# Performance work log

Hardware: AMD Instinct MI355X
Metric: run time of the kernel (lower is better)

## Reference

```python
import jax, jax.numpy as jnp
import numpy as np


def _conv(x, w, b, stride=1):
    # torch Conv2d(kernel=3, padding=1) in NCHW / OIHW layout
    y = jax.lax.conv_general_dilated(x, w, (stride, stride), ((1, 1), (1, 1)),
                                     dimension_numbers=('NCHW', 'OIHW', 'NCHW'))
    return y + b[None, :, None, None]


def _up2(x):
    # nn.Upsample(scale_factor=2, mode='nearest')
    return jnp.repeat(jnp.repeat(x, 2, axis=2), 2, axis=3)


def _decode(z, fc_w, fc_b, w1, b1, w2, b2, w3, b3):
    # ConvDecoderMid: fc -> [B,32,7,7] -> up -> elu(conv) -> up -> elu(conv) -> sigmoid(conv)
    B = z.shape[0]
    h = (z @ fc_w + fc_b).reshape(B, 32, 7, 7)
    h = _up2(h)
    h = jax.nn.elu(_conv(h, w1, b1))
    h = _up2(h)
    h = jax.nn.elu(_conv(h, w2, b2))
    return jax.nn.sigmoid(_conv(h, w3, b3))  # [B,1,28,28]


def setup_inputs() -> dict:
    key = jax.random.key(0)
    B, L, E = 2048, 64, 8
    ks = jax.random.split(key, 16)
    rn = lambda k, s, sc: jax.random.normal(k, s, dtype=jnp.float32) * sc
    p = {}
    p['x'] = jax.random.uniform(ks[0], (B, 1, 28, 28), dtype=jnp.float32)
    p['eps'] = jax.random.normal(ks[1], (B, L), dtype=jnp.float32)
    # ConvEncoder
    p['enc_w1'] = rn(ks[2], (32, 1, 3, 3), 0.3);  p['enc_b1'] = jnp.zeros((32,), jnp.float32)
    p['enc_w2'] = rn(ks[3], (64, 32, 3, 3), 0.06); p['enc_b2'] = jnp.zeros((64,), jnp.float32)
    p['enc_w3'] = rn(ks[4], (128, 64, 3, 3), 0.04); p['enc_b3'] = jnp.zeros((128,), jnp.float32)
    p['w_mu'] = rn(ks[5], (128 * 7 * 7, L), 0.01); p['b_mu'] = jnp.zeros((L,), jnp.float32)
    p['w_lv'] = rn(ks[6], (128 * 7 * 7, L), 0.01); p['b_lv'] = jnp.zeros((L,), jnp.float32)
    # GatingNetwork
    p['g_w1'] = rn(ks[7], (L, 64), 0.1); p['g_b1'] = jnp.zeros((64,), jnp.float32)
    p['g_w2'] = rn(ks[8], (64, 32), 0.1); p['g_b2'] = jnp.zeros((32,), jnp.float32)
    p['g_w3'] = rn(ks[9], (32, E), 0.1); p['g_b3'] = jnp.zeros((E,), jnp.float32)
    # E ConvDecoderMid experts, params stacked on leading expert axis
    p['d_fc_w'] = rn(ks[10], (E, L, 32 * 7 * 7), 0.05); p['d_fc_b'] = jnp.zeros((E, 32 * 7 * 7), jnp.float32)
    p['d_w1'] = rn(ks[11], (E, 64, 32, 3, 3), 0.06); p['d_b1'] = jnp.zeros((E, 64), jnp.float32)
    p['d_w2'] = rn(ks[12], (E, 32, 64, 3, 3), 0.04); p['d_b2'] = jnp.zeros((E, 32), jnp.float32)
    p['d_w3'] = rn(ks[13], (E, 1, 32, 3, 3), 0.06); p['d_b3'] = jnp.zeros((E, 1), jnp.float32)
    return p


def reference(x, eps, enc_w1, enc_b1, enc_w2, enc_b2, enc_w3, enc_b3,
              w_mu, b_mu, w_lv, b_lv,
              g_w1, g_b1, g_w2, g_b2, g_w3, g_b3,
              d_fc_w, d_fc_b, d_w1, d_b1, d_w2, d_b2, d_w3, d_b3):
    B = x.shape[0]
    # encoder: 28 -> 28 -> 14 -> 7
    h = jax.nn.relu(_conv(x, enc_w1, enc_b1))
    h = jax.nn.relu(_conv(h, enc_w2, enc_b2, stride=2))
    h = jax.nn.relu(_conv(h, enc_w3, enc_b3, stride=2))
    h = h.reshape(B, -1)  # [B, 6272]
    mu = h @ w_mu + b_mu
    log_var = h @ w_lv + b_lv
    z = mu + eps * jnp.exp(0.5 * log_var)
    # gating
    g = jax.nn.relu(z @ g_w1 + g_b1)
    g = jax.nn.relu(g @ g_w2 + g_b2)
    expert_probs = jax.nn.softmax(g @ g_w3 + g_b3, axis=-1)
    expert_indices = jnp.argmax(expert_probs, axis=-1)  # [B]
    # run ALL experts on full batch (faithful to original), stack [E,B,1,28,28]
    all_rec = jax.vmap(_decode, in_axes=(None, 0, 0, 0, 0, 0, 0, 0, 0))(
        z, d_fc_w, d_fc_b, d_w1, d_b1, d_w2, d_b2, d_w3, d_b3)
    reconstructed_x = all_rec[expert_indices, jnp.arange(B)]  # [B,1,28,28]
    logits = jnp.log(expert_probs + 1e-8)
    return (reconstructed_x, mu, log_var, logits, expert_probs)
```

## Files before the change

kernel.cpp:

```cpp
#include <hip/hip_runtime.h>
#include <hip/hip_bf16.h>


#define NB 2048

typedef short bf16x8 __attribute__((ext_vector_type(8)));
typedef float f32x4  __attribute__((ext_vector_type(4)));
typedef unsigned u32x4 __attribute__((ext_vector_type(4)));

static constexpr int OFF_RECON  = 0;
static constexpr int OFF_MU     = 1605632;
static constexpr int OFF_LV     = 1736704;
static constexpr int OFF_LOGITS = 1867776;
static constexpr int OFF_PROBS  = 1884160;

static constexpr size_t WS_U    = 0;
static constexpr size_t WS_Z    = 25690112;
static constexpr size_t WS_IDX  = 25821184;
static constexpr size_t WS_WENC = 25821696;
static constexpr size_t W2S_OFF = 0;
static constexpr size_t W3S_OFF = 36864;
static constexpr size_t WFC_OFF = 184320;
static constexpr size_t HFC_OFF = 0;
static constexpr size_t W1B_OFF = 17000448;
static constexpr size_t WCB_OFF = 17074176;

__device__ __forceinline__ float relu_f(float v) { return v > 0.f ? v : 0.f; }
__device__ __forceinline__ float elu_f(float v)  {
  return __expf(fminf(v, 0.f)) - 1.f + fmaxf(v, 0.f);
}
__device__ __forceinline__ short f2b(float v) {
  __hip_bfloat16 h = __float2bfloat16(v);
  short s; __builtin_memcpy(&s, &h, 2); return s;
}
__device__ __forceinline__ float s2f(short s) {
  unsigned v = ((unsigned)(unsigned short)s) << 16;
  float f; __builtin_memcpy(&f, &v, 4); return f;
}
__device__ __forceinline__ unsigned pack2(float v) {
  short h = f2b(v);
  short m = f2b(v - s2f(h));
  return (unsigned)(unsigned short)h | ((unsigned)(unsigned short)m << 16);
}

__global__ __launch_bounds__(256) void k_prep_enc(
    const float* __restrict__ ew2, const float* __restrict__ ew3,
    const float* __restrict__ wmu, const float* __restrict__ wlv,
    unsigned short* __restrict__ w2s, unsigned short* __restrict__ w3s,
    unsigned* __restrict__ wfc)
{
  const int u = blockIdx.x * 256 + threadIdx.x;
  if (u >= 894976) return;
  if (u >= 92160) {
    const int u2 = u - 92160;
    const int kp = u2 >> 8, r = u2 & 255;
    const int n = r >> 1, j = r & 1;
    const int k = kp * 2 + j;
    const float w = (n < 64) ? wmu[k * 64 + n] : wlv[k * 64 + (n - 64)];
    short h = f2b(w);
    short mm = f2b(w - s2f(h));
    wfc[u2] = (unsigned)(unsigned short)h | ((unsigned)(unsigned short)mm << 16);
    return;
  }
  float w; uint2* dst;
  if (u < 18432) {
    int ic = u & 7, oc = (u >> 3) & 63;
    int r = u >> 9;
    int tap = r % 9, chunk = r / 9;
    w = ew2[oc * 288 + (chunk * 8 + ic) * 9 + tap];
    dst = (uint2*)w2s + u;
  } else {
    int u2 = u - 18432;
    int ic = u2 & 7, oc = (u2 >> 3) & 127;
    int r = u2 >> 10;
    int tap = r % 9, chunk = r / 9;
    w = ew3[oc * 576 + (chunk * 8 + ic) * 9 + tap];
    dst = (uint2*)w3s + u2;
  }
  short h = f2b(w);
  short mm = f2b(w - s2f(h));
  uint2 pk;
  pk.x = (unsigned)(unsigned short)h | ((unsigned)(unsigned short)mm << 16);
  pk.y = (unsigned)(unsigned short)h | ((unsigned)(unsigned short)h << 16);
  *dst = pk;
}

__global__ __launch_bounds__(512, 4) void k_enc(
    const float* __restrict__ x,
    const float* __restrict__ w1, const float* __restrict__ b1,
    const float* __restrict__ b2g, const unsigned short* __restrict__ w2s,
    const unsigned short* __restrict__ w3s, const float* __restrict__ b3,
    unsigned* __restrict__ hb)
{
  __shared__ float sX[900];
  __shared__ float sB2[64];
  __shared__ float sB3[128];
  __shared__ __align__(16) short sH[36000];

  const int n = blockIdx.x, t = threadIdx.x;

  for (int idx = t; idx < 900; idx += 512) {
    int yy = idx / 30, xx = idx % 30;
    float v = 0.f;
    if (yy >= 1 && yy <= 28 && xx >= 1 && xx <= 28)
      v = x[n * 784 + (yy - 1) * 28 + (xx - 1)];
    sX[idx] = v;
  }
  if (t < 64) sB2[t] = b2g[t];
  if (t >= 64 && t < 192) sB3[t - 64] = b3[t - 64];
  for (int bi = t; bi < 116; bi += 512) {
    int p;
    if (bi < 30) p = bi;
    else if (bi < 60) p = 870 + (bi - 30);
    else if (bi < 88) p = (bi - 59) * 30;
    else p = (bi - 87) * 30 + 29;
    unsigned* d = (unsigned*)&sH[p * 40];
    #pragma unroll
    for (int j = 0; j < 20; ++j) d[j] = 0u;
  }
  __syncthreads();

  float xw[2][9];
  int hp[2]; bool pvld[2];
  #pragma unroll
  for (int i = 0; i < 2; ++i) {
    int p = t + 512 * i;
    pvld[i] = (p < 784);
    int yy = pvld[i] ? p / 28 : 0, xx = pvld[i] ? p % 28 : 0;
    hp[i] = (yy + 1) * 30 + xx + 1;
    #pragma unroll
    for (int k = 0; k < 9; ++k)
      xw[i][k] = sX[(yy + k / 3) * 30 + xx + (k % 3)];
  }

  const int lane = t & 63, wv = t >> 6;
  const int q = lane >> 4, m16 = lane & 15;
  const int nth = wv & 1, mh = wv >> 1;
  const int nm = (mh == 0) ? 4 : 3;

  int abase[4];
  #pragma unroll
  for (int mtl = 0; mtl < 4; ++mtl) {
    int m = (mh + 4 * mtl) * 16 + m16; if (m > 195) m = 195;
    int yy = m / 14, xx = m % 14;
    abase[mtl] = (yy * 60 + xx * 2) * 40 + q * 8;
  }
  f32x4 acc[4][2];
  #pragma unroll
  for (int a = 0; a < 4; ++a) { acc[a][0] = (f32x4)0.f; acc[a][1] = (f32x4)0.f; }

  for (int c = 0; c < 4; ++c) {
    #pragma unroll
    for (int o = 0; o < 8; ++o) {
      const int oc = c * 8 + o;
      float wr[9];
      #pragma unroll
      for (int k = 0; k < 9; ++k) wr[k] = w1[oc * 9 + k];
      const float bb = b1[oc];
      #pragma unroll
      for (int i = 0; i < 2; ++i) if (pvld[i]) {
        float v = bb;
        #pragma unroll
        for (int k = 0; k < 9; ++k) v += xw[i][k] * wr[k];
        v = relu_f(v);
        short h = f2b(v); float hf = s2f(h);
        short mm = f2b(v - hf); float mf = s2f(mm);
        short ll = f2b(v - hf - mf);
        uint2 pk;
        pk.x = (unsigned)(unsigned short)h | ((unsigned)(unsigned short)h << 16);
        pk.y = (unsigned)(unsigned short)mm | ((unsigned)(unsigned short)ll << 16);
        *(uint2*)&sH[hp[i] * 40 + o * 4] = pk;
      }
    }
    __syncthreads();

    const unsigned short* wb = w2s + (size_t)c * 18432;
    for (int tap = 0; tap < 9; ++tap) {
      const int toff = ((tap / 3) * 30 + (tap % 3)) * 40;
      bf16x8 A[4];
      #pragma unroll
      for (int mtl = 0; mtl < 4; ++mtl)
        A[mtl] = *(const bf16x8*)&sH[abase[mtl] + toff];
      #pragma unroll
      for (int ntl = 0; ntl < 2; ++ntl) {
        const int ocl = nth * 32 + ntl * 16 + m16;
        bf16x8 B = *(const bf16x8*)&wb[(tap * 64 + ocl) * 32 + q * 8];
        #pragma unroll
        for (int mtl = 0; mtl < 4; ++mtl)
          if (mtl < nm)
            acc[mtl][ntl] = __builtin_amdgcn_mfma_f32_16x16x32_bf16(A[mtl], B, acc[mtl][ntl], 0, 0, 0);
      }
    }
    __syncthreads();
  }

  unsigned* h2p = (unsigned*)sH;
  short* sIn = sH + 25600;
  #pragma unroll
  for (int mtl = 0; mtl < 4; ++mtl) {
    if (mtl < nm) {
      const int mt = mh + 4 * mtl;
      #pragma unroll
      for (int ntl = 0; ntl < 2; ++ntl) {
        const int oc = nth * 32 + ntl * 16 + m16;
        const float bb = sB2[oc];
        #pragma unroll
        for (int r = 0; r < 4; ++r) {
          int p = mt * 16 + q * 4 + r;
          if (p < 196)
            h2p[p * 65 + oc] = pack2(relu_f(acc[mtl][ntl][r] + bb));
        }
      }
    }
  }
  for (int bi = t; bi < 60; bi += 512) {
    int p;
    if (bi < 16) p = bi;
    else if (bi < 32) p = 240 + (bi - 16);
    else if (bi < 46) p = (bi - 31) * 16;
    else p = (bi - 45) * 16 + 15;
    unsigned* d = (unsigned*)&sIn[p * 40];
    #pragma unroll
    for (int j = 0; j < 20; ++j) d[j] = 0u;
  }

  const int oc3 = wv * 16 + m16;
  int abase3[4];
  #pragma unroll
  for (int mtl = 0; mtl < 4; ++mtl) {
    int m = mtl * 16 + m16; if (m > 48) m = 48;
    int yy = m / 7, xx = m % 7;
    abase3[mtl] = (yy * 32 + xx * 2) * 40 + q * 8;
  }
  f32x4 acc3[4];
  #pragma unroll
  for (int a = 0; a < 4; ++a) acc3[a] = (f32x4)0.f;

  for (int c = 0; c < 8; ++c) {
    __syncthreads();
    if (t < 392) {
      int pix = t >> 1, icoff = (t & 1) * 4;
      int rr = pix / 14 + 1, cc = pix % 14 + 1;
      short* drow = &sIn[(rr * 16 + cc) * 40 + icoff * 4];
      #pragma unroll
      for (int i = 0; i < 4; ++i) {
        unsigned u = h2p[pix * 65 + c * 8 + icoff + i];
        uint2 pk;
        pk.x = (u << 16) | (u & 0xffffu);
        pk.y = u >> 16;
        *(uint2*)&drow[i * 4] = pk;
      }
    }
    __syncthreads();

    const unsigned short* wc = w3s + (size_t)c * 36864;
    for (int tap = 0; tap < 9; ++tap) {
      const int toff = ((tap / 3) * 16 + (tap % 3)) * 40;
      bf16x8 B = *(const bf16x8*)&wc[(tap * 128 + oc3) * 32 + q * 8];
      #pragma unroll
      for (int mtl = 0; mtl < 4; ++mtl) {
        bf16x8 A = *(const bf16x8*)&sIn[abase3[mtl] + toff];
        acc3[mtl] = __builtin_amdgcn_mfma_f32_16x16x32_bf16(A, B, acc3[mtl], 0, 0, 0);
      }
    }
  }

  const float bb3 = sB3[oc3];
  #pragma unroll
  for (int mtl = 0; mtl < 4; ++mtl) {
    #pragma unroll
    for (int r = 0; r < 4; ++r) {
      int m = mtl * 16 + q * 4 + r;
      if (m < 49)
        hb[(size_t)n * 12544 + oc3 * 49 + m] = pack2(relu_f(acc3[mtl][r] + bb3));
    }
  }
}

__global__ __launch_bounds__(256) void k_fc(
    const unsigned* __restrict__ A2,
    const unsigned* __restrict__ wfc,
    float* __restrict__ Uf)
{
  const int t = threadIdx.x;
  const int lane = t & 63, wv = t >> 6;
  const int q = lane >> 4, m16 = lane & 15;
  const int m0 = blockIdx.x * 64;
  const int s  = blockIdx.y;

  const unsigned* arow[4];
  #pragma unroll
  for (int mt = 0; mt < 4; ++mt)
    arow[mt] = A2 + (size_t)(m0 + mt * 16 + m16) * 12544 + s * 784 + 2 * q;
  const unsigned* brow[2];
  #pragma unroll
  for (int ntl = 0; ntl < 2; ++ntl)
    brow[ntl] = wfc + (size_t)(s * 392 + q) * 256 + ((wv * 2 + ntl) * 16 + m16) * 2;

  f32x4 acc[4][2];
  #pragma unroll
  for (int a = 0; a < 4; ++a) { acc[a][0] = (f32x4)0.f; acc[a][1] = (f32x4)0.f; }

  #pragma unroll 2
  for (int kt = 0; kt < 98; ++kt) {
    bf16x8 Af[4];
    #pragma unroll
    for (int mt = 0; mt < 4; ++mt) {
      uint2 u = *(const uint2*)(arow[mt] + kt * 8);
      u32x4 w = { (u.x << 16) | (u.x & 0xffffu), u.x >> 16,
                  (u.y << 16) | (u.y & 0xffffu), u.y >> 16 };
      Af[mt] = __builtin_bit_cast(bf16x8, w);
    }
    #pragma unroll
    for (int ntl = 0; ntl < 2; ++ntl) {
      uint2 u = *(const uint2*)(brow[ntl] + kt * 1024);
      u32x4 w = { u.x, (u.x << 16) | (u.x & 0xffffu),
                  u.y, (u.y << 16) | (u.y & 0xffffu) };
      bf16x8 Bf = __builtin_bit_cast(bf16x8, w);
      #pragma unroll
      for (int mt = 0; mt < 4; ++mt)
        acc[mt][ntl] = __builtin_amdgcn_mfma_f32_16x16x32_bf16(Af[mt], Bf, acc[mt][ntl], 0, 0, 0);
    }
  }

  #pragma unroll
  for (int mt = 0; mt < 4; ++mt) {
    #pragma unroll
    for (int ntl = 0; ntl < 2; ++ntl) {
      const int n = (wv * 2 + ntl) * 16 + m16;
      #pragma unroll
      for (int r = 0; r < 4; ++r) {
        const int row = m0 + mt * 16 + q * 4 + r;
        Uf[(size_t)row * 12544 + 6272 + s * 128 + n] = acc[mt][ntl][r];
      }
    }
  }
}

__global__ __launch_bounds__(256) void k_gate(
    const float* __restrict__ Ubase,
    const float* __restrict__ b_mu, const float* __restrict__ b_lv,
    const float* __restrict__ eps,
    const float* __restrict__ gw1, const float* __restrict__ gb1,
    const float* __restrict__ gw2, const float* __restrict__ gb2,
    const float* __restrict__ gw3, const float* __restrict__ gb3,
    float* __restrict__ out, float* __restrict__ zbuf, int* __restrict__ idxbuf)
{
  __shared__ float sZ[4][64];
  __shared__ float sG1[4][64];
  __shared__ float sG2[4][32];
  const int t = threadIdx.x;
  const int wv = t >> 6, lane = t & 63;
  const int m = blockIdx.x * 4 + wv;
  const float* __restrict__ Up = Ubase + (size_t)m * 12544 + 6272;

  {
    const int k = lane;
    float mu = b_mu[k], lv = b_lv[k];
    #pragma unroll
    for (int s8 = 0; s8 < 8; ++s8) {
      mu += Up[s8 * 128 + k];
      lv += Up[s8 * 128 + 64 + k];
    }
    out[OFF_MU + m * 64 + k] = mu;
    out[OFF_LV + m * 64 + k] = lv;
    float zz = mu + eps[m * 64 + k] * expf(0.5f * lv);
    sZ[wv][k] = zz;
    zbuf[m * 64 + k] = zz;
  }

  {
    const int j = lane;
    float a = gb1[j];
    for (int k = 0; k < 64; ++k) a += sZ[wv][k] * gw1[k * 64 + j];
    sG1[wv][j] = relu_f(a);
  }
  if (lane < 32) {
    const int j = lane;
    float a = gb2[j];
    for (int k = 0; k < 64; ++k) a += sG1[wv][k] * gw2[k * 32 + j];
    sG2[wv][j] = relu_f(a);
  }
  float l = -1e30f;
  if (lane < 8) {
    float a = gb3[lane];
    for (int k = 0; k < 32; ++k) a += sG2[wv][k] * gw3[k * 8 + lane];
    l = a;
  }
  float mx = l;
  #pragma unroll
  for (int off = 4; off; off >>= 1) mx = fmaxf(mx, __shfl_xor(mx, off, 8));
  float p = expf(l - mx);
  float ssum = p;
  #pragma unroll
  for (int off = 4; off; off >>= 1) ssum += __shfl_xor(ssum, off, 8);
  float pj = p / ssum;
  if (lane < 8) {
    out[OFF_PROBS + m * 8 + lane] = pj;
    out[OFF_LOGITS + m * 8 + lane] = logf(pj + 1e-8f);
  }
  float pmax = pj;
  #pragma unroll
  for (int off = 4; off; off >>= 1) pmax = fmaxf(pmax, __shfl_xor(pmax, off, 8));
  unsigned long long msk = __ballot(lane < 8 && pj == pmax);
  if (lane == 0) idxbuf[m] = __ffsll(msk) - 1;
}

__global__ __launch_bounds__(256) void k_prep(
    const float* __restrict__ dw1, const float* __restrict__ dw2,
    unsigned short* __restrict__ w1b, unsigned short* __restrict__ wcb)
{
  const int e = blockIdx.x, job = blockIdx.y, t = threadIdx.x;
  if (job == 0) {
    for (int idx = t; idx < 18432; idx += 256) {
      int tap = idx >> 11;
      int rem = idx & 2047;
      int octile = rem >> 9;
      int lane = (rem >> 3) & 63;
      int j = idx & 7;
      int oc = octile * 16 + (lane & 15);
      int ic = (lane >> 4) * 8 + j;
      w1b[(size_t)e * 18432 + idx] =
          (unsigned short)f2b(dw1[(size_t)e * 18432 + (oc * 32 + ic) * 9 + tap]);
    }
  } else {
    const int par = job - 1, py = par >> 1, px = par & 1;
    for (int v = t; v < 8192; v += 256) {
      int s = v >> 10;
      int nt = (v >> 9) & 1;
      int lane = (v >> 3) & 63;
      int j = v & 7;
      int oc = nt * 16 + (lane & 15);
      int tap = s >> 1, h = s & 1;
      int ty = tap >> 1, tx = tap & 1;
      int icg = h * 32 + (lane >> 4) * 8 + j;
      int ys = (ty == 0) ? 0 : (1 + py);
      int yc = (ty == py) ? 1 : 2;
      int xs = (tx == 0) ? 0 : (1 + px);
      int xc = (tx == px) ? 1 : 2;
      const float* wp = &dw2[(size_t)e * 18432 + (oc * 64 + icg) * 9];
      float a = 0.f;
      for (int ky = ys; ky < ys + yc; ++ky)
        for (int kx = xs; kx < xs + xc; ++kx)
          a += wp[ky * 3 + kx];
      wcb[((size_t)e * 4 + par) * 8192 + v] = (unsigned short)f2b(a);
    }
  }
}

__global__ __launch_bounds__(256) void k_dfc(
    const float* __restrict__ zbuf, const int* __restrict__ idxbuf,
    const float* __restrict__ fcw, const float* __restrict__ fcb,
    unsigned* __restrict__ hfcb)
{
  __shared__ float sZ[64];
  __shared__ __align__(16) unsigned short sO[1568];
  const int n = blockIdx.x, t = threadIdx.x;
  const int e = idxbuf[n];
  if (t < 64) sZ[t] = zbuf[n * 64 + t];
  __syncthreads();
  const float* __restrict__ W = fcw + (size_t)e * 100352;
  const int i40 = t, i41 = t + 256;
  const bool v1 = (i41 < 392);
  float a0[4], a1[4];
  {
    float4 b0 = *(const float4*)&fcb[e * 1568 + i40 * 4];
    a0[0] = b0.x; a0[1] = b0.y; a0[2] = b0.z; a0[3] = b0.w;
    if (v1) {
      float4 b1v = *(const float4*)&fcb[e * 1568 + i41 * 4];
      a1[0] = b1v.x; a1[1] = b1v.y; a1[2] = b1v.z; a1[3] = b1v.w;
    } else { a1[0] = a1[1] = a1[2] = a1[3] = 0.f; }
  }
  for (int k = 0; k < 64; ++k) {
    const float zk = sZ[k];
    float4 w0 = *(const float4*)&W[k * 1568 + i40 * 4];
    a0[0] += zk * w0.x; a0[1] += zk * w0.y; a0[2] += zk * w0.z; a0[3] += zk * w0.w;
    if (v1) {
      float4 w1v = *(const float4*)&W[k * 1568 + i41 * 4];
      a1[0] += zk * w1v.x; a1[1] += zk * w1v.y; a1[2] += zk * w1v.z; a1[3] += zk * w1v.w;
    }
  }
  #pragma unroll
  for (int c = 0; c < 4; ++c) {
    int j = i40 * 4 + c;
    int ic = j / 49, p = j % 49;
    sO[p * 32 + ic] = (unsigned short)f2b(a0[c]);
  }
  if (v1) {
    #pragma unroll
    for (int c = 0; c < 4; ++c) {
      int j = i41 * 4 + c;
      int ic = j / 49, p = j % 49;
      sO[p * 32 + ic] = (unsigned short)f2b(a1[c]);
    }
  }
  __syncthreads();
  for (int idx = t; idx < 784; idx += 256)
    hfcb[(size_t)n * 784 + idx] = ((const unsigned*)sO)[idx];
}

__global__ __launch_bounds__(512, 4) void k_dec(
    const unsigned* __restrict__ hfcb, const int* __restrict__ idxbuf,
    const unsigned* __restrict__ w1b, const float* __restrict__ db1,
    const unsigned* __restrict__ wcb, const float* __restrict__ b2,
    const float* __restrict__ w3, const float* __restrict__ b3,
    float* __restrict__ out)
{
  __shared__ __align__(16) short sPool[32712];
  __shared__ float sB1[64];
  __shared__ float sB2[32];

  short* sInH  = sPool;
  short* sW    = sPool + 10240;
  short* sD1   = sPool + 10240;
  short* sU    = sPool;
  short* sW3b  = sPool + 28672;
  float* sC    = (float*)(sPool + 29184);

  const int n = blockIdx.x, t = threadIdx.x;
  const int e = idxbuf[n];

  {
    int cell = t >> 1, half = t & 1;
    int r = cell >> 4, c = cell & 15;
    bool inter = (r >= 1 && r <= 14 && c >= 1 && c <= 14);
    int src = inter ? (((r - 1) >> 1) * 7 + ((c - 1) >> 1)) : 0;
    const unsigned* hp = &hfcb[(size_t)n * 784 + src * 16 + half * 8];
    unsigned* dst = (unsigned*)&sInH[cell * 40] + half * 8;
    #pragma unroll
    for (int i = 0; i < 8; ++i) dst[i] = inter ? hp[i] : 0u;
  }
  {
    const unsigned* wsrc = w1b + (size_t)e * 9216;
    unsigned* wd = (unsigned*)sW;
    for (int idx = t; idx < 9216; idx += 512) wd[idx] = wsrc[idx];
  }
  {
    int nn = t >> 5, k = t & 31;
    if (t < 512) sW3b[t] = (nn < 9) ? f2b(w3[e * 288 + k * 9 + nn]) : (short)0;
  }
  if (t < 64) sB1[t] = db1[e * 64 + t];
  if (t >= 64 && t < 96) sB2[t - 64] = b2[e * 32 + (t - 64)];
  __syncthreads();

  const int wv = t >> 6, lane = t & 63;
  const int q = lane >> 4, m16 = lane & 15;

  {
    const int octile = wv & 3, mh2 = wv >> 2;
    const int ocl = octile * 16 + m16;
    const int nmA = (mh2 == 0) ? 7 : 6;

    f32x4 accA[7];
    int abA[7];
    #pragma unroll
    for (int i = 0; i < 7; ++i) {
      accA[i] = (f32x4)0.f;
      int mt = mh2 + 2 * i; if (mt > 12) mt = 12;
      int p = mt * 16 + m16; if (p > 195) p = 195;
      int y = p / 14, x = p % 14;
      abA[i] = (y * 16 + x) * 40 + q * 8;
    }

    for (int tap = 0; tap < 9; ++tap) {
      const int toff = ((tap / 3) * 16 + (tap % 3)) * 40;
      bf16x8 bfrag = *(const bf16x8*)&sW[tap * 2048 + octile * 512 + lane * 8];
      #pragma unroll
      for (int i = 0; i < 7; ++i) {
        if (i < nmA) {
          bf16x8 afrag = *(const bf16x8*)&sInH[abA[i] + toff];
          accA[i] = __builtin_amdgcn_mfma_f32_16x16x32_bf16(afrag, bfrag, accA[i], 0, 0, 0);
        }
      }
    }
    __syncthreads();

    for (int v = t; v < 1920; v += 512) {
      int bi = v >> 5, j = v & 31;
      int p;
      if (bi < 16) p = bi;
      else if (bi < 32) p = 240 + (bi - 16);
      else if (bi < 46) p = (bi - 31) * 16;
      else p = (bi - 45) * 16 + 15;
      ((unsigned*)&sD1[p * 72])[j] = 0u;
    }
    const float bias = sB1[ocl];
    #pragma unroll
    for (int i = 0; i < 7; ++i) {
      if (i < nmA) {
        int mt = mh2 + 2 * i;
        #pragma unroll
        for (int r = 0; r < 4; ++r) {
          int p = mt * 16 + q * 4 + r;
          if (p < 196) {
            int row = p / 14, col = p % 14;
            sD1[((row + 1) * 16 + col + 1) * 72 + ocl] =
                f2b(elu_f(accA[i][r] + bias));
          }
        }
      }
    }
  }
  __syncthreads();

  const int nt = wv & 1, mh = wv >> 1;
  const int ocl = nt * 16 + m16;
  const int nm = (mh == 0) ? 4 : 3;

  const bf16x8 b3f = *(const bf16x8*)&sW3b[m16 * 32 + q * 8];

  int mt3[2], ab3[2];
  const int nmt3 = (wv < 5) ? 2 : 1;
  #pragma unroll
  for (int i = 0; i < 2; ++i) {
    int mt = wv + 8 * i; if (mt > 12) mt = 12;
    mt3[i] = mt;
    int p = mt * 16 + m16; if (p > 195) p = 195;
    ab3[i] = p * 40 + q * 8;
  }

  int PY[2], PX[2];
  #pragma unroll
  for (int g = 0; g < 2; ++g) {
    int P = t + 512 * g;
    PY[g] = (P < 784) ? P / 28 : -100;
    PX[g] = (P < 784) ? P % 28 : 0;
  }
  float racc[2] = {0.f, 0.f};

  int ab0[4];
  #pragma unroll
  for (int im = 0; im < 4; ++im) {
    int mt = mh + 4 * im;
    int p = mt * 16 + m16; if (p > 195) p = 195;
    int a = p / 14, bb = p % 14;
    ab0[im] = (a * 16 + bb) * 72 + q * 8;
  }

  for (int par = 0; par < 4; ++par) {
    const int py = par >> 1, px = par & 1;

    {
      const unsigned* wc = wcb + ((size_t)e * 4 + par) * 4096;
      unsigned* du = (unsigned*)sU;
      for (int v = t; v < 4096; v += 512) du[v] = wc[v];
    }
    __syncthreads();

    f32x4 acc[4];
    #pragma unroll
    for (int im = 0; im < 4; ++im) acc[im] = (f32x4)0.f;
    const int pbase = (py * 16 + px) * 72;
    for (int s = 0; s < 8; ++s) {
      int tap = s >> 1, h = s & 1;
      int ty = tap >> 1, tx = tap & 1;
      int toff = pbase + (ty * 16 + tx) * 72 + h * 32;
      bf16x8 bfrag = *(const bf16x8*)&sU[s * 1024 + nt * 512 + lane * 8];
      #pragma unroll
      for (int im = 0; im < 4; ++im) {
        if (im < nm) {
          bf16x8 afrag = *(const bf16x8*)&sD1[ab0[im] + toff];
          acc[im] = __builtin_amdgcn_mfma_f32_16x16x32_bf16(afrag, bfrag, acc[im], 0, 0, 0);
        }
      }
    }
    __syncthreads();

    {
      const float bias = sB2[ocl];
      #pragma unroll
      for (int im = 0; im < 4; ++im) {
        if (im < nm) {
          int mt = mh + 4 * im;
          #pragma unroll
          for (int r = 0; r < 4; ++r) {
            int p = mt * 16 + q * 4 + r;
            if (p < 196) sU[p * 40 + ocl] = f2b(elu_f(acc[im][r] + bias));
          }
        }
      }
    }
    __syncthreads();

    #pragma unroll
    for (int i = 0; i < 2; ++i) {
      if (i < nmt3) {
        bf16x8 af = *(const bf16x8*)&sU[ab3[i]];
        f32x4 a3 = (f32x4)0.f;
        a3 = __builtin_amdgcn_mfma_f32_16x16x32_bf16(af, b3f, a3, 0, 0, 0);
        if (m16 < 9) {
          #pragma unroll
          for (int r = 0; r < 4; ++r) {
            int p = mt3[i] * 16 + q * 4 + r;
            if (p < 196) sC[p * 9 + m16] = a3[r];
          }
        }
      }
    }
    __syncthreads();

    #pragma unroll
    for (int g = 0; g < 2; ++g) {
      const int Y = PY[g], X = PX[g];
      if (Y < 0) continue;
      int RS[2]; int nr = 0;
      if ((Y & 1) == py) { RS[0] = Y; nr = 1; }
      else { if (Y > 0) RS[nr++] = Y - 1; if (Y < 27) RS[nr++] = Y + 1; }
      int CS[2]; int nc = 0;
      if ((X & 1) == px) { CS[0] = X; nc = 1; }
      else { if (X > 0) CS[nc++] = X - 1; if (X < 27) CS[nc++] = X + 1; }
      float s = 0.f;
      for (int ir = 0; ir < nr; ++ir) {
        const int R = RS[ir];
        const int a = (R - py) >> 1, ky = R - Y + 1;
        for (int jc = 0; jc < nc; ++jc) {
          const int C = CS[jc];
          const int bq = (C - px) >> 1, kx = C - X + 1;
          s += sC[(a * 14 + bq) * 9 + ky * 3 + kx];
        }
      }
      racc[g] += s;
    }
    __syncthreads();
  }

  const float b3e = b3[e];
  #pragma unroll
  for (int g = 0; g < 2; ++g) {
    int P = t + 512 * g;
    if (P < 784)
      out[OFF_RECON + (size_t)n * 784 + P] = 1.f / (1.f + __expf(-(racc[g] + b3e)));
  }
}

extern "C" void kernel_launch(void* const* d_in, const int* in_sizes, int n_in,
                              void* d_out, int out_size, void* d_ws, size_t ws_size,
                              hipStream_t stream) {
  const float* x    = (const float*)d_in[0];
  const float* eps  = (const float*)d_in[1];
  const float* ew1  = (const float*)d_in[2];
  const float* eb1  = (const float*)d_in[3];
  const float* ew2  = (const float*)d_in[4];
  const float* eb2  = (const float*)d_in[5];
  const float* ew3  = (const float*)d_in[6];
  const float* eb3  = (const float*)d_in[7];
  const float* wmu  = (const float*)d_in[8];
  const float* bmu  = (const float*)d_in[9];
  const float* wlv  = (const float*)d_in[10];
  const float* blv  = (const float*)d_in[11];
  const float* gw1  = (const float*)d_in[12];
  const float* gb1  = (const float*)d_in[13];
  const float* gw2  = (const float*)d_in[14];
  const float* gb2  = (const float*)d_in[15];
  const float* gw3  = (const float*)d_in[16];
  const float* gb3  = (const float*)d_in[17];
  const float* dfcw = (const float*)d_in[18];
  const float* dfcb = (const float*)d_in[19];
  const float* dw1  = (const float*)d_in[20];
  const float* db1  = (const float*)d_in[21];
  const float* dw2  = (const float*)d_in[22];
  const float* db2  = (const float*)d_in[23];
  const float* dw3  = (const float*)d_in[24];
  const float* db3  = (const float*)d_in[25];

  float* out = (float*)d_out;
  float* ws  = (float*)d_ws;

  float* U    = ws + WS_U;
  float* zb   = ws + WS_Z;
  int*   idx  = (int*)(ws + WS_IDX);
  unsigned* hfcb = (unsigned*)(U + HFC_OFF);
  unsigned short* w1b = (unsigned short*)(U + W1B_OFF);
  unsigned short* wcb = (unsigned short*)(U + WCB_OFF);
  unsigned short* w2s = (unsigned short*)(ws + WS_WENC + W2S_OFF);
  unsigned short* w3s = (unsigned short*)(ws + WS_WENC + W3S_OFF);
  unsigned* wfc = (unsigned*)(ws + WS_WENC + WFC_OFF);

  k_prep_enc<<<3496, 256, 0, stream>>>(ew2, ew3, wmu, wlv, w2s, w3s, wfc);
  k_enc   <<<NB, 512, 0, stream>>>(x, ew1, eb1, eb2, w2s, w3s, eb3, (unsigned*)U);
  k_fc    <<<dim3(32, 8), 256, 0, stream>>>((const unsigned*)U, wfc, U);
  k_gate  <<<512, 256, 0, stream>>>(U, bmu, blv, eps, gw1, gb1, gw2, gb2, gw3, gb3,
                                    out, zb, idx);
  k_prep  <<<dim3(8, 5), 256, 0, stream>>>(dw1, dw2, w1b, wcb);
  k_dfc   <<<NB, 256, 0, stream>>>(zb, idx, dfcw, dfcb, hfcb);
  k_dec   <<<NB, 512, 0, stream>>>(hfcb, idx, (const unsigned*)w1b, db1,
                                   (const unsigned*)wcb, db2, dw3, db3, out);
}
```

Before: 519.7 us.

## Split shared-memory activation tiles by column parity; drop third bf16 split term

```diff
diff --git a/kernel.cpp b/kernel.cpp
--- a/kernel.cpp
+++ b/kernel.cpp
@@ -114,7 +114,8 @@
     else if (bi < 60) p = 870 + (bi - 30);
     else if (bi < 88) p = (bi - 59) * 30;
     else p = (bi - 87) * 30 + 29;
-    unsigned* d = (unsigned*)&sH[p * 40];
+    int row = p / 30, col = p % 30;
+    unsigned* d = (unsigned*)&sH[row * 1200 + (col & 1) * 600 + (col >> 1) * 40];
     #pragma unroll
     for (int j = 0; j < 20; ++j) d[j] = 0u;
   }
@@ -127,7 +128,8 @@
     int p = t + 512 * i;
     pvld[i] = (p < 784);
     int yy = pvld[i] ? p / 28 : 0, xx = pvld[i] ? p % 28 : 0;
-    hp[i] = (yy + 1) * 30 + xx + 1;
+    int row = yy + 1, col = xx + 1;
+    hp[i] = row * 1200 + (col & 1) * 600 + (col >> 1) * 40;
     #pragma unroll
     for (int k = 0; k < 9; ++k)
       xw[i][k] = sX[(yy + k / 3) * 30 + xx + (k % 3)];
@@ -143,7 +145,7 @@
   for (int mtl = 0; mtl < 4; ++mtl) {
     int m = (mh + 4 * mtl) * 16 + m16; if (m > 195) m = 195;
     int yy = m / 14, xx = m % 14;
-    abase[mtl] = (yy * 60 + xx * 2) * 40 + q * 8;
+    abase[mtl] = yy * 2400 + xx * 40 + q * 8;
   }
   f32x4 acc[4][2];
   #pragma unroll
@@ -163,20 +165,20 @@
         #pragma unroll
         for (int k = 0; k < 9; ++k) v += xw[i][k] * wr[k];
         v = relu_f(v);
-        short h = f2b(v); float hf = s2f(h);
-        short mm = f2b(v - hf); float mf = s2f(mm);
-        short ll = f2b(v - hf - mf);
+        short h = f2b(v);
+        short mm = f2b(v - s2f(h));
         uint2 pk;
         pk.x = (unsigned)(unsigned short)h | ((unsigned)(unsigned short)h << 16);
-        pk.y = (unsigned)(unsigned short)mm | ((unsigned)(unsigned short)ll << 16);
-        *(uint2*)&sH[hp[i] * 40 + o * 4] = pk;
+        pk.y = (unsigned)(unsigned short)mm;
+        *(uint2*)&sH[hp[i] + o * 4] = pk;
       }
     }
     __syncthreads();
 
     const unsigned short* wb = w2s + (size_t)c * 18432;
     for (int tap = 0; tap < 9; ++tap) {
-      const int toff = ((tap / 3) * 30 + (tap % 3)) * 40;
+      const int ty = tap / 3, tx = tap % 3;
+      const int toff = ty * 1200 + (tx & 1) * 600 + (tx >> 1) * 40;
       bf16x8 A[4];
       #pragma unroll
       for (int mtl = 0; mtl < 4; ++mtl)
@@ -219,7 +221,8 @@
     else if (bi < 32) p = 240 + (bi - 16);
     else if (bi < 46) p = (bi - 31) * 16;
     else p = (bi - 45) * 16 + 15;
-    unsigned* d = (unsigned*)&sIn[p * 40];
+    int row = p >> 4, col = p & 15;
+    unsigned* d = (unsigned*)&sIn[row * 640 + (col & 1) * 320 + (col >> 1) * 40];
     #pragma unroll
     for (int j = 0; j < 20; ++j) d[j] = 0u;
   }
@@ -230,7 +233,7 @@
   for (int mtl = 0; mtl < 4; ++mtl) {
     int m = mtl * 16 + m16; if (m > 48) m = 48;
     int yy = m / 7, xx = m % 7;
-    abase3[mtl] = (yy * 32 + xx * 2) * 40 + q * 8;
+    abase3[mtl] = yy * 1280 + xx * 40 + q * 8;
   }
   f32x4 acc3[4];
   #pragma unroll
@@ -241,7 +244,7 @@
     if (t < 392) {
       int pix = t >> 1, icoff = (t & 1) * 4;
       int rr = pix / 14 + 1, cc = pix % 14 + 1;
-      short* drow = &sIn[(rr * 16 + cc) * 40 + icoff * 4];
+      short* drow = &sIn[rr * 640 + (cc & 1) * 320 + (cc >> 1) * 40 + icoff * 4];
       #pragma unroll
       for (int i = 0; i < 4; ++i) {
         unsigned u = h2p[pix * 65 + c * 8 + icoff + i];
@@ -255,7 +258,8 @@
 
     const unsigned short* wc = w3s + (size_t)c * 36864;
     for (int tap = 0; tap < 9; ++tap) {
-      const int toff = ((tap / 3) * 16 + (tap % 3)) * 40;
+      const int ty = tap / 3, tx = tap % 3;
+      const int toff = ty * 640 + (tx & 1) * 320 + (tx >> 1) * 40;
       bf16x8 B = *(const bf16x8*)&wc[(tap * 128 + oc3) * 32 + q * 8];
       #pragma unroll
       for (int mtl = 0; mtl < 4; ++mtl) {
```

Result: slower. 536.6 us (+3.3%).
